# Performance work log

Hardware: AMD Instinct MI355X
Metric: run time of the kernel (lower is better)

Reference implementation:

```python
import jax, jax.numpy as jnp
import numpy as np

N_HEADS = 32
N_KV_HEADS = 8
HEAD_DIM = 64
ROPE_BASE = 10000.0


def _rope(t):
    # t: [b, s, h, d]; Llama-style rotate-half RoPE
    b, s, h, d = t.shape
    inv_freq = 1.0 / (ROPE_BASE ** (jnp.arange(0, d, 2, dtype=jnp.float32) / d))
    freqs = jnp.arange(s, dtype=jnp.float32)[:, None] * inv_freq[None, :]  # [s, d/2]
    cos = jnp.cos(freqs)[None, :, None, :].astype(t.dtype)
    sin = jnp.sin(freqs)[None, :, None, :].astype(t.dtype)
    t1, t2 = t[..., : d // 2], t[..., d // 2 :]
    return jnp.concatenate([t1 * cos - t2 * sin, t2 * cos + t1 * sin], axis=-1)


def setup_inputs() -> dict:
    key = jax.random.key(0)
    ks = jax.random.split(key, 5)
    b, s, d = 2, 2048, 2048
    dkv = d // (N_HEADS // N_KV_HEADS)
    sc = 1.0 / np.sqrt(d)
    return {
        "x": jax.random.normal(ks[0], (b, s, d), jnp.float32),
        "wq": jax.random.normal(ks[1], (d, d), jnp.float32) * sc,
        "wk": jax.random.normal(ks[2], (d, dkv), jnp.float32) * sc,
        "wv": jax.random.normal(ks[3], (d, dkv), jnp.float32) * sc,
        "wo": jax.random.normal(ks[4], (d, d), jnp.float32) * sc,
    }


def reference(x, wq, wk, wv, wo):
    b, s, d = x.shape
    g = N_HEADS // N_KV_HEADS
    q = (x @ wq).reshape(b, s, N_HEADS, HEAD_DIM)
    k = (x @ wk).reshape(b, s, N_KV_HEADS, HEAD_DIM)
    v = (x @ wv).reshape(b, s, N_KV_HEADS, HEAD_DIM)
    q = _rope(q)
    k = _rope(k)
    # GQA: repeat kv heads to match query heads
    k = jnp.repeat(k, g, axis=2)  # [b, s, N_HEADS, d_h]
    v = jnp.repeat(v, g, axis=2)
    scale = 1.0 / np.sqrt(HEAD_DIM)
    scores = jnp.einsum("bqhd,bkhd->bhqk", q, k) * scale  # [b, h, s, s]
    causal = jnp.tril(jnp.ones((s, s), dtype=bool))
    scores = jnp.where(causal[None, None], scores, jnp.finfo(scores.dtype).min)
    probs = jax.nn.softmax(scores, axis=-1)
    out = jnp.einsum("bhqk,bkhd->bqhd", probs, v).reshape(b, s, d)
    return out @ wo
```

## Files before the change

kernel.cpp:

```cpp
#include <hip/hip_runtime.h>
#include <hip/hip_bf16.h>
#include <stdint.h>

typedef __attribute__((ext_vector_type(8))) __bf16 bf16x8;
typedef __attribute__((ext_vector_type(4))) __bf16 bf16x4;
typedef __attribute__((ext_vector_type(4))) float f32x4;

#define QSCALE (0.125f * 1.44269504f)

#define GL16(src, dst) __builtin_amdgcn_global_load_lds( \
    (const __attribute__((address_space(1))) void*)(src), \
    (__attribute__((address_space(3))) void*)(dst), 16, 0, 0)

static __device__ inline unsigned pkbf(float a, float b) {
  __bf16 x = (__bf16)a, y = (__bf16)b;
  unsigned short ux = __builtin_bit_cast(unsigned short, x);
  unsigned short uy = __builtin_bit_cast(unsigned short, y);
  return ((unsigned)uy << 16) | ux;
}

static __device__ inline float ex2(float x) {
#if __has_builtin(__builtin_amdgcn_exp2f)
  return __builtin_amdgcn_exp2f(x);
#else
  float r;
  asm("v_exp_f32 %0, %1" : "=v"(r) : "v"(x));
  return r;
#endif
}

__global__ __launch_bounds__(256) void k_prep(const float* __restrict__ x,
                                              __bf16* __restrict__ xb,
                                              const float* __restrict__ wq,
                                              const float* __restrict__ wk,
                                              const float* __restrict__ wv,
                                              const float* __restrict__ wo,
                                              __bf16* __restrict__ wqkvT,
                                              __bf16* __restrict__ woT,
                                              float* __restrict__ ct,
                                              float* __restrict__ st) {
  int bid = blockIdx.x, tid = threadIdx.x;
  if (bid < 4096) {
    int i = bid * 256 + tid;
    const float4* p = (const float4*)(x) + (size_t)i * 2;
    float4 a = p[0], b = p[1];
    bf16x8 o;
    o[0] = (__bf16)a.x; o[1] = (__bf16)a.y; o[2] = (__bf16)a.z; o[3] = (__bf16)a.w;
    o[4] = (__bf16)b.x; o[5] = (__bf16)b.y; o[6] = (__bf16)b.z; o[7] = (__bf16)b.w;
    ((bf16x8*)xb)[i] = o;
    return;
  }
  if (bid >= 14336) {
    int i = (bid - 14336) * 256 + tid;
    int s = i >> 5, j = i & 31;
    float invf = powf(10000.0f, -(float)j / 32.0f);
    float fr = (float)s * invf;
    ct[i] = cosf(fr);
    st[i] = sinf(fr);
    return;
  }
  __shared__ float tile[32][33];
  const float* w;
  __bf16* wT;
  int N, r;
  if (bid < 8192)       { r = bid - 4096;  w = wq; wT = wqkvT;                        N = 2048; }
  else if (bid < 9216)  { r = bid - 8192;  w = wk; wT = wqkvT + (size_t)2048 * 2048;  N = 512; }
  else if (bid < 10240) { r = bid - 9216;  w = wv; wT = wqkvT + (size_t)2560 * 2048;  N = 512; }
  else                  { r = bid - 10240; w = wo; wT = woT;                          N = 2048; }
  int ntiles = N >> 5;
  int n0 = (r % ntiles) * 32, k0 = (r / ntiles) * 32;
  int tx = tid & 31, ty = tid >> 5;
#pragma unroll
  for (int i = 0; i < 32; i += 8)
    tile[ty + i][tx] = w[(size_t)(k0 + ty + i) * N + n0 + tx];
  __syncthreads();
#pragma unroll
  for (int i = 0; i < 32; i += 8)
    wT[(size_t)(n0 + ty + i) * 2048 + k0 + tx] = (__bf16)tile[tx][ty + i];
}

template <int BN, int NW, int WPN, int MODE>
__global__ __launch_bounds__(NW * 64, NW / 4) void k_gemm256(const __bf16* __restrict__ A,
                                                             const __bf16* __restrict__ BT,
                                                             void* __restrict__ C0,
                                                             __bf16* __restrict__ kb,
                                                             __bf16* __restrict__ vt,
                                                             const float* __restrict__ ct,
                                                             const float* __restrict__ st,
                                                             int K, int NBN) {
  constexpr int WPM = NW / WPN;
  constexpr int MF = 256 / WPM / 16;
  constexpr int NF = BN / WPN / 16;
  constexpr int MH = MF / 2;
  constexpr int CHA = 256 * 8;
  constexpr int CHB = BN * 8;
  constexpr int PA = CHA / (NW * 64);
  constexpr int RA = CHA - PA * NW * 64;
  constexpr int PB = CHB / (NW * 64);
  static_assert(CHB % (NW * 64) == 0, "B chunks must tile threads");
  static_assert(RA % 64 == 0, "A remainder must be wave-aligned");
  static_assert(NF == 4, "epilogue assumes 64-col wave window");
  __shared__ __align__(16) __bf16 lA[2][256 * 64];
  __shared__ __align__(16) __bf16 lB[2][BN * 64];
  int bm = (blockIdx.x / NBN) << 8;
  int bn = (blockIdx.x % NBN) * BN;
  int tid = threadIdx.x, l = tid & 63, w = tid >> 6;
  int wr = w / WPN, wc = w % WPN;
  int lrow = l & 15, lk = l >> 4;
  int NT = K >> 6;
  f32x4 acc[MF][NF] = {};

#define STG(T, BUF)                                                           \
  do {                                                                        \
    int k0_ = (T) << 6;                                                       \
    _Pragma("unroll") for (int i_ = 0; i_ < PA; i_++) {                       \
      int ch_ = i_ * (NW * 64) + tid;                                         \
      int r_ = ch_ >> 3, c_ = ch_ & 7;                                        \
      GL16(A + (size_t)(bm + r_) * K + k0_ + ((c_ ^ (r_ & 7)) << 3),          \
           &lA[BUF][(i_ * (NW * 64) + (w << 6)) * 8]);                        \
    }                                                                         \
    if constexpr (RA > 0) {                                                   \
      if (tid < RA) {                                                         \
        int ch_ = PA * (NW * 64) + tid;                                       \
        int r_ = ch_ >> 3, c_ = ch_ & 7;                                      \
        GL16(A + (size_t)(bm + r_) * K + k0_ + ((c_ ^ (r_ & 7)) << 3),        \
             &lA[BUF][(PA * (NW * 64) + (w << 6)) * 8]);                      \
      }                                                                       \
    }                                                                         \
    _Pragma("unroll") for (int i_ = 0; i_ < PB; i_++) {                       \
      int ch_ = i_ * (NW * 64) + tid;                                         \
      int r_ = ch_ >> 3, c_ = ch_ & 7;                                        \
      GL16(BT + (size_t)(bn + r_) * K + k0_ + ((c_ ^ (r_ & 7)) << 3),         \
           &lB[BUF][(i_ * (NW * 64) + (w << 6)) * 8]);                        \
    }                                                                         \
  } while (0)

#define WAITN()                                                               \
  do {                                                                        \
    if constexpr (RA > 0) {                                                   \
      if (w < (RA >> 6))                                                      \
        asm volatile("s_waitcnt vmcnt(%0)" ::"i"(PA + PB + 1) : "memory");    \
      else                                                                    \
        asm volatile("s_waitcnt vmcnt(%0)" ::"i"(PA + PB) : "memory");        \
    } else {                                                                  \
      asm volatile("s_waitcnt vmcnt(%0)" ::"i"(PA + PB) : "memory");          \
    }                                                                         \
  } while (0)

  STG(0, 0);
  STG(1, 1);
  WAITN();
  __builtin_amdgcn_sched_barrier(0);
  __builtin_amdgcn_s_barrier();

  for (int t = 0; t < NT; t++) {
    int buf = t & 1;
    const char* bA = (const char*)lA[buf];
    const char* bB = (const char*)lB[buf];
    bf16x8 bfr[NF][2], af0[MH][2], af1[MH][2];
#pragma unroll
    for (int nf = 0; nf < NF; nf++) {
      int row = wc * (NF * 16) + nf * 16 + lrow;
#pragma unroll
      for (int kc = 0; kc < 2; kc++)
        bfr[nf][kc] = *(const bf16x8*)(bB + row * 128 +
                                       ((kc * 64 + 16 * lk) ^ ((row & 7) << 4)));
    }
#pragma unroll
    for (int mf = 0; mf < MH; mf++) {
      int row = wr * (MF * 16) + mf * 16 + lrow;
#pragma unroll
      for (int kc = 0; kc < 2; kc++)
        af0[mf][kc] = *(const bf16x8*)(bA + row * 128 +
                                       ((kc * 64 + 16 * lk) ^ ((row & 7) << 4)));
    }
    __builtin_amdgcn_s_setprio(1);
#pragma unroll
    for (int kc = 0; kc < 2; kc++)
#pragma unroll
      for (int mf = 0; mf < MH; mf++)
#pragma unroll
        for (int nf = 0; nf < NF; nf++)
          acc[mf][nf] = __builtin_amdgcn_mfma_f32_16x16x32_bf16(af0[mf][kc], bfr[nf][kc],
                                                                acc[mf][nf], 0, 0, 0);
    __builtin_amdgcn_s_setprio(0);
#pragma unroll
    for (int mf = 0; mf < MH; mf++) {
      int row = wr * (MF * 16) + (MH + mf) * 16 + lrow;
#pragma unroll
      for (int kc = 0; kc < 2; kc++)
        af1[mf][kc] = *(const bf16x8*)(bA + row * 128 +
                                       ((kc * 64 + 16 * lk) ^ ((row & 7) << 4)));
    }
    asm volatile("s_waitcnt lgkmcnt(0)" ::: "memory");
    __builtin_amdgcn_sched_barrier(0);
    __builtin_amdgcn_s_barrier();
    if (t + 2 < NT) STG(t + 2, buf);
    __builtin_amdgcn_s_setprio(1);
#pragma unroll
    for (int kc = 0; kc < 2; kc++)
#pragma unroll
      for (int mf = 0; mf < MH; mf++)
#pragma unroll
        for (int nf = 0; nf < NF; nf++)
          acc[MH + mf][nf] = __builtin_amdgcn_mfma_f32_16x16x32_bf16(
              af1[mf][kc], bfr[nf][kc], acc[MH + mf][nf], 0, 0, 0);
    __builtin_amdgcn_s_setprio(0);
    if (t + 2 < NT) {
      WAITN();
    } else {
      asm volatile("s_waitcnt vmcnt(0)" ::: "memory");
    }
    __builtin_amdgcn_sched_barrier(0);
    __builtin_amdgcn_s_barrier();
  }
#undef STG
#undef WAITN

  if constexpr (MODE == 0) {
    int wcb = bn + wc * 64;
    __bf16* qb = (__bf16*)C0;
    if (wcb < 2048) {
#pragma unroll
      for (int mf = 0; mf < MF; mf++)
#pragma unroll
        for (int r = 0; r < 4; r++) {
          int row = bm + wr * (MF * 16) + mf * 16 + 4 * lk + r;
          int sidx = row & 2047;
#pragma unroll
          for (int nfl = 0; nfl < 2; nfl++) {
            int d = nfl * 16 + lrow;
            float c = ct[sidx * 32 + d], sn = st[sidx * 32 + d];
            float a = acc[mf][nfl][r], b2 = acc[mf][nfl + 2][r];
            qb[(size_t)row * 2048 + wcb + d] = (__bf16)((a * c - b2 * sn) * QSCALE);
            qb[(size_t)row * 2048 + wcb + d + 32] = (__bf16)((b2 * c + a * sn) * QSCALE);
          }
        }
    } else if (wcb < 2560) {
      int cb = wcb - 2048;
#pragma unroll
      for (int mf = 0; mf < MF; mf++)
#pragma unroll
        for (int r = 0; r < 4; r++) {
          int row = bm + wr * (MF * 16) + mf * 16 + 4 * lk + r;
          int sidx = row & 2047;
#pragma unroll
          for (int nfl = 0; nfl < 2; nfl++) {
            int d = nfl * 16 + lrow;
            float c = ct[sidx * 32 + d], sn = st[sidx * 32 + d];
            float a = acc[mf][nfl][r], b2 = acc[mf][nfl + 2][r];
            kb[(size_t)row * 512 + cb + d] = (__bf16)(a * c - b2 * sn);
            kb[(size_t)row * 512 + cb + d + 32] = (__bf16)(b2 * c + a * sn);
          }
        }
    } else {
      int hkk = (wcb - 2560) >> 6;
#pragma unroll
      for (int mf = 0; mf < MF; mf++)
#pragma unroll
        for (int nf = 0; nf < NF; nf++)
#pragma unroll
          for (int r = 0; r < 4; r++) {
            int row = bm + wr * (MF * 16) + mf * 16 + 4 * lk + r;
            int dd = nf * 16 + lrow;
            int bb = row >> 11, s = row & 2047;
            vt[(size_t)(((bb << 3) + hkk) * 64 + dd) * 2048 + s] = (__bf16)acc[mf][nf][r];
          }
    }
  } else {
    float* C = (float*)C0;
#pragma unroll
    for (int mf = 0; mf < MF; mf++)
#pragma unroll
      for (int nf = 0; nf < NF; nf++)
#pragma unroll
        for (int r = 0; r < 4; r++) {
          int row = bm + wr * (MF * 16) + mf * 16 + 4 * lk + r;
          int col = bn + wc * 64 + nf * 16 + lrow;
          C[(size_t)row * 2048 + col] = acc[mf][nf][r];
        }
  }
}

template <int BN, int NW, int WPN, int MODE>
__global__ __launch_bounds__(NW * 64, NW / 4) void k_gemm3d(const __bf16* __restrict__ A,
                                                            const __bf16* __restrict__ BT,
                                                            void* __restrict__ C0,
                                                            int K, int NBN) {
  constexpr int WPM = NW / WPN;
  constexpr int MF = 256 / WPM / 16;
  constexpr int NF = BN / WPN / 16;
  constexpr int MH = MF / 2;
  constexpr int CHA = 256 * 8;
  constexpr int CHB = BN * 8;
  constexpr int PA = CHA / (NW * 64);
  constexpr int RA = CHA - PA * NW * 64;
  constexpr int PB = CHB / (NW * 64);
  static_assert(CHB % (NW * 64) == 0, "B chunks must tile threads");
  static_assert(RA % 64 == 0, "A remainder must be wave-aligned");
  static_assert(NF == 4, "wave owns a 64-col window");
  constexpr int LB = PB;
  constexpr int LA0 = PA + (RA > 0 ? 1 : 0);
  constexpr int LA1 = PA;
  constexpr int NS0 = 2 * LA0 + LB, NS1 = 2 * LA1 + LB;
  constexpr int NM0 = LA0 + LB, NM1 = LA1 + LB;
  __shared__ __align__(16) __bf16 lA[3][256 * 64];
  __shared__ __align__(16) __bf16 lB[2][BN * 64];
  int bid = blockIdx.x;
  int lg = (bid & 7) * ((int)gridDim.x >> 3) + (bid >> 3);
  int bm = (lg / NBN) << 8;
  int bn = (lg % NBN) * BN;
  int tid = threadIdx.x, l = tid & 63, w = tid >> 6;
  int wr = w / WPN, wc = w % WPN;
  int lrow = l & 15, lk = l >> 4;
  int NT = K >> 6;
  f32x4 acc[MF][NF] = {};

#define STGA(T, BUF)                                                          \
  do {                                                                        \
    int k0_ = (T) << 6;                                                       \
    _Pragma("unroll") for (int i_ = 0; i_ < PA; i_++) {                       \
      int ch_ = i_ * (NW * 64) + tid;                                         \
      int r_ = ch_ >> 3, c_ = ch_ & 7;                                        \
      GL16(A + (size_t)(bm + r_) * K + k0_ + ((c_ ^ (r_ & 7)) << 3),          \
           &lA[BUF][(i_ * (NW * 64) + (w << 6)) * 8]);                        \
    }                                                                         \
    if constexpr (RA > 0) {                                                   \
      if (tid < RA) {                                                         \
        int ch_ = PA * (NW * 64) + tid;                                       \
        int r_ = ch_ >> 3, c_ = ch_ & 7;                                      \
        GL16(A + (size_t)(bm + r_) * K + k0_ + ((c_ ^ (r_ & 7)) << 3),        \
             &lA[BUF][(PA * (NW * 64) + (w << 6)) * 8]);                      \
      }                                                                       \
    }                                                                         \
  } while (0)

#define STGB(T, BUF)                                                          \
  do {                                                                        \
    int k0_ = (T) << 6;                                                       \
    _Pragma("unroll") for (int i_ = 0; i_ < PB; i_++) {                       \
      int ch_ = i_ * (NW * 64) + tid;                                         \
      int r_ = ch_ >> 3, c_ = ch_ & 7;                                        \
      GL16(BT + (size_t)(bn + r_) * K + k0_ + ((c_ ^ (r_ & 7)) << 3),         \
           &lB[BUF][(i_ * (NW * 64) + (w << 6)) * 8]);                        \
    }                                                                         \
  } while (0)

#define WAIT_STEADY()                                                         \
  do {                                                                        \
    if constexpr (RA > 0) {                                                   \
      if (w < (RA >> 6))                                                      \
        asm volatile("s_waitcnt vmcnt(%0)" ::"i"(NS0) : "memory");            \
      else                                                                    \
        asm volatile("s_waitcnt vmcnt(%0)" ::"i"(NS1) : "memory");            \
    } else {                                                                  \
      asm volatile("s_waitcnt vmcnt(%0)" ::"i"(NS1) : "memory");              \
    }                                                                         \
  } while (0)

#define WAIT_MID()                                                            \
  do {                                                                        \
    if constexpr (RA > 0) {                                                   \
      if (w < (RA >> 6))                                                      \
        asm volatile("s_waitcnt vmcnt(%0)" ::"i"(NM0) : "memory");            \
      else                                                                    \
        asm volatile("s_waitcnt vmcnt(%0)" ::"i"(NM1) : "memory");            \
    } else {                                                                  \
      asm volatile("s_waitcnt vmcnt(%0)" ::"i"(NM1) : "memory");              \
    }                                                                         \
  } while (0)

  STGB(0, 0); STGA(0, 0);
  STGB(1, 1); STGA(1, 1);
  STGA(2, 2);
  WAIT_STEADY();
  __builtin_amdgcn_sched_barrier(0);
  __builtin_amdgcn_s_barrier();

  int a0 = 0;
  for (int t = 0; t < NT; t++) {
    const char* bA = (const char*)lA[a0];
    const char* bB = (const char*)lB[t & 1];
    bf16x8 bfr[NF][2], af0[MH][2], af1[MH][2];
#pragma unroll
    for (int nf = 0; nf < NF; nf++) {
      int row = wc * (NF * 16) + nf * 16 + lrow;
#pragma unroll
      for (int kc = 0; kc < 2; kc++)
        bfr[nf][kc] = *(const bf16x8*)(bB + row * 128 +
                                       ((kc * 64 + 16 * lk) ^ ((row & 7) << 4)));
    }
#pragma unroll
    for (int mf = 0; mf < MH; mf++) {
      int row = wr * (MF * 16) + mf * 16 + lrow;
#pragma unroll
      for (int kc = 0; kc < 2; kc++)
        af0[mf][kc] = *(const bf16x8*)(bA + row * 128 +
                                       ((kc * 64 + 16 * lk) ^ ((row & 7) << 4)));
    }
#pragma unroll
    for (int mf = 0; mf < MH; mf++) {
      int row = wr * (MF * 16) + (MH + mf) * 16 + lrow;
#pragma unroll
      for (int kc = 0; kc < 2; kc++)
        af1[mf][kc] = *(const bf16x8*)(bA + row * 128 +
                                       ((kc * 64 + 16 * lk) ^ ((row & 7) << 4)));
    }
    __builtin_amdgcn_s_setprio(1);
#pragma unroll
    for (int kc = 0; kc < 2; kc++)
#pragma unroll
      for (int mf = 0; mf < MH; mf++)
#pragma unroll
        for (int nf = 0; nf < NF; nf++)
          acc[mf][nf] = __builtin_amdgcn_mfma_f32_16x16x32_bf16(af0[mf][kc], bfr[nf][kc],
                                                                acc[mf][nf], 0, 0, 0);
    __builtin_amdgcn_s_setprio(0);
    asm volatile("s_waitcnt lgkmcnt(0)" ::: "memory");
    __builtin_amdgcn_sched_barrier(0);
    __builtin_amdgcn_s_barrier();
    if (t + 2 < NT) STGB(t + 2, t & 1);
    if (t + 3 < NT) STGA(t + 3, a0);
    __builtin_amdgcn_s_setprio(1);
#pragma unroll
    for (int kc = 0; kc < 2; kc++)
#pragma unroll
      for (int mf = 0; mf < MH; mf++)
#pragma unroll
        for (int nf = 0; nf < NF; nf++)
          acc[MH + mf][nf] = __builtin_amdgcn_mfma_f32_16x16x32_bf16(
              af1[mf][kc], bfr[nf][kc], acc[MH + mf][nf], 0, 0, 0);
    __builtin_amdgcn_s_setprio(0);
    if (t + 3 < NT) {
      WAIT_STEADY();
    } else if (t + 2 < NT) {
      WAIT_MID();
    } else if (t + 1 < NT) {
      asm volatile("s_waitcnt vmcnt(0)" ::: "memory");
    }
    __builtin_amdgcn_sched_barrier(0);
    __builtin_amdgcn_s_barrier();
    a0 = (a0 == 2) ? 0 : a0 + 1;
  }
#undef STGA
#undef STGB
#undef WAIT_STEADY
#undef WAIT_MID

  float* C = (float*)C0;
#pragma unroll
  for (int mf = 0; mf < MF; mf++)
#pragma unroll
    for (int nf = 0; nf < NF; nf++)
#pragma unroll
      for (int r = 0; r < 4; r++) {
        int row = bm + wr * (MF * 16) + mf * 16 + 4 * lk + r;
        int col = bn + wc * 64 + nf * 16 + lrow;
        C[(size_t)row * 2048 + col] = acc[mf][nf][r];
      }
}

__global__ __launch_bounds__(256, 3) void k_attn(const __bf16* __restrict__ Q,
                                                 const __bf16* __restrict__ Kb,
                                                 const __bf16* __restrict__ VT,
                                                 __bf16* __restrict__ O) {
  __shared__ __align__(16) __bf16 lK[2][64 * 64];
  __shared__ __align__(16) __bf16 lV[2][64 * 64];
  int bid = blockIdx.x;
  int g = bid >> 8, k = (bid >> 4) & 15;
  int c;
  if (g == 0) c = 63 - k;
  else if (g == 1) c = 32 + k;
  else if (g == 2) c = 31 - k;
  else c = k;
  int hk = bid & 7;
  int b = (bid >> 3) & 1;
  int tid = threadIdx.x, l = tid & 63, w = tid >> 6;
  int h = hk * 4 + w;
  int lrow = l & 15, lk = l >> 4;
  int sw = (lrow & 7) << 4;
  int tl = c >> 1;

#define STAGE(BUF, T)                                                                     \
  do {                                                                                    \
    int kv0_ = (T) * 64;                                                                  \
    _Pragma("unroll") for (int i_ = 0; i_ < 2; i_++) {                                    \
      int cb_ = i_ * 256 + w * 64;                                                        \
      int chunk_ = cb_ + l;                                                               \
      int row_ = chunk_ >> 3, cc_ = chunk_ & 7;                                           \
      GL16(Kb + (size_t)(b * 2048 + kv0_ + row_) * 512 + hk * 64 +                        \
               ((cc_ ^ (row_ & 7)) << 3),                                                 \
           &lK[BUF][cb_ * 8]);                                                            \
      GL16(VT + (size_t)((b * 8 + hk) * 64 + row_) * 2048 + kv0_ +                        \
               ((cc_ ^ (row_ & 7)) << 3),                                                 \
           &lV[BUF][cb_ * 8]);                                                            \
    }                                                                                     \
  } while (0)

  bf16x8 aq[2][2];
#pragma unroll
  for (int qf = 0; qf < 2; qf++) {
    int qrow = c * 32 + qf * 16 + lrow;
    const __bf16* qp = Q + (size_t)(b * 2048 + qrow) * 2048 + h * 64 + lk * 8;
    aq[qf][0] = *(const bf16x8*)qp;
    aq[qf][1] = *(const bf16x8*)(qp + 32);
  }
  f32x4 o[2][4] = {};
  float lp[2] = {0.f, 0.f};
  STAGE(0, 0);
  for (int t = 0, buf = 0; t <= tl; t++, buf ^= 1) {
    asm volatile("s_waitcnt vmcnt(0)" ::: "memory");
    __syncthreads();
    if (t < tl) STAGE(buf ^ 1, t + 1);
    const char* K_ = (const char*)lK[buf];
    const char* V_ = (const char*)lV[buf];
    f32x4 s4[2][4];
    __builtin_amdgcn_s_setprio(1);
#pragma unroll
    for (int nf = 0; nf < 4; nf++) {
      const char* kr = K_ + (nf * 16 + lrow) * 128;
      bf16x8 bk0 = *(const bf16x8*)(kr + ((16 * lk) ^ sw));
      bf16x8 bk1 = *(const bf16x8*)(kr + ((64 + 16 * lk) ^ sw));
#pragma unroll
      for (int qf = 0; qf < 2; qf++) {
        f32x4 z = {};
        z = __builtin_amdgcn_mfma_f32_16x16x32_bf16(bk0, aq[qf][0], z, 0, 0, 0);
        z = __builtin_amdgcn_mfma_f32_16x16x32_bf16(bk1, aq[qf][1], z, 0, 0, 0);
        s4[qf][nf] = z;
      }
    }
    __builtin_amdgcn_s_setprio(0);
    if (t == tl) {
      int qo = (c & 1) * 32;
#pragma unroll
      for (int qf = 0; qf < 2; qf++) {
        int qoff = qo + qf * 16 + lrow;
#pragma unroll
        for (int nf = 0; nf < 4; nf++)
#pragma unroll
          for (int r = 0; r < 4; r++)
            if (nf * 16 + 4 * lk + r > qoff) s4[qf][nf][r] = -1e30f;
      }
    }
#pragma unroll
    for (int qf = 0; qf < 2; qf++) {
      float ps = 0.f;
#pragma unroll
      for (int nf = 0; nf < 4; nf++)
#pragma unroll
        for (int r = 0; r < 4; r++) {
          float pv = ex2(s4[qf][nf][r]);
          s4[qf][nf][r] = pv;
          ps += pv;
        }
      lp[qf] += ps;
    }
    __builtin_amdgcn_s_setprio(1);
#pragma unroll
    for (int np = 0; np < 2; np++) {
      bf16x8 pb[2];
#pragma unroll
      for (int qf = 0; qf < 2; qf++) {
        uint4 t4;
        t4.x = pkbf(s4[qf][np][0], s4[qf][np][1]);
        t4.y = pkbf(s4[qf][np][2], s4[qf][np][3]);
        t4.z = pkbf(s4[qf][np + 2][0], s4[qf][np + 2][1]);
        t4.w = pkbf(s4[qf][np + 2][2], s4[qf][np + 2][3]);
        pb[qf] = __builtin_bit_cast(bf16x8, t4);
      }
#pragma unroll
      for (int dn = 0; dn < 4; dn++) {
        const char* vr = V_ + (dn * 16 + lrow) * 128;
        uint2 a0 = *(const uint2*)(vr + ((np * 32 + 8 * lk) ^ sw));
        uint2 a1 = *(const uint2*)(vr + (((np + 2) * 32 + 8 * lk) ^ sw));
        uint4 av;
        av.x = a0.x; av.y = a0.y; av.z = a1.x; av.w = a1.y;
        bf16x8 va = __builtin_bit_cast(bf16x8, av);
#pragma unroll
        for (int qf = 0; qf < 2; qf++)
          o[qf][dn] = __builtin_amdgcn_mfma_f32_16x16x32_bf16(va, pb[qf], o[qf][dn], 0, 0, 0);
      }
    }
    __builtin_amdgcn_s_setprio(0);
  }
#pragma unroll
  for (int qf = 0; qf < 2; qf++) {
    float s = lp[qf];
    s += __shfl_xor(s, 16);
    s += __shfl_xor(s, 32);
    float inv = 1.f / s;
    int qrow = c * 32 + qf * 16 + lrow;
    __bf16* op = O + (size_t)(b * 2048 + qrow) * 2048 + h * 64 + 4 * lk;
#pragma unroll
    for (int dn = 0; dn < 4; dn++) {
      bf16x4 stv;
#pragma unroll
      for (int r = 0; r < 4; r++) stv[r] = (__bf16)(o[qf][dn][r] * inv);
      *(bf16x4*)(op + dn * 16) = stv;
    }
  }
#undef STAGE
}

extern "C" void kernel_launch(void* const* d_in, const int* in_sizes, int n_in,
                              void* d_out, int out_size, void* d_ws, size_t ws_size,
                              hipStream_t stream) {
  const float* x = (const float*)d_in[0];
  const float* wq = (const float*)d_in[1];
  const float* wk = (const float*)d_in[2];
  const float* wv = (const float*)d_in[3];
  const float* wo = (const float*)d_in[4];
  char* ws = (char*)d_ws;
  __bf16* xb    = (__bf16*)(ws + 0);
  __bf16* wqkvT = (__bf16*)(ws + 16777216);
  __bf16* woT   = (__bf16*)(ws + 29360128);
  __bf16* qb    = (__bf16*)(ws + 37748736);
  __bf16* kb    = (__bf16*)(ws + 54525952);
  __bf16* vt    = (__bf16*)(ws + 58720256);
  __bf16* ob    = (__bf16*)(ws + 62914560);
  float*  ct    = (float*)(ws + 79691776);
  float*  st    = (float*)(ws + 79953920);
  float* out = (float*)d_out;

  k_prep<<<14592, 256, 0, stream>>>(x, xb, wq, wk, wv, wo, wqkvT, woT, ct, st);
  k_gemm256<192, 12, 3, 0><<<256, 768, 0, stream>>>(xb, wqkvT, qb, kb, vt, ct, st, 2048, 16);
  k_attn<<<1024, 256, 0, stream>>>(qb, kb, vt, ob);
  k_gemm3d<128, 8, 2, 1><<<256, 512, 0, stream>>>(ob, woT, out, 2048, 16);
}
```

Before: 162.3 us.

## Fuse fp32-to-bf16 conversion of x into QKV GEMM A-tile loads

```diff
diff --git a/kernel.cpp b/kernel.cpp
--- a/kernel.cpp
+++ b/kernel.cpp
@@ -29,9 +29,7 @@
 #endif
 }
 
-__global__ __launch_bounds__(256) void k_prep(const float* __restrict__ x,
-                                              __bf16* __restrict__ xb,
-                                              const float* __restrict__ wq,
+__global__ __launch_bounds__(256) void k_prep(const float* __restrict__ wq,
                                               const float* __restrict__ wk,
                                               const float* __restrict__ wv,
                                               const float* __restrict__ wo,
@@ -40,18 +38,8 @@
                                               float* __restrict__ ct,
                                               float* __restrict__ st) {
   int bid = blockIdx.x, tid = threadIdx.x;
-  if (bid < 4096) {
-    int i = bid * 256 + tid;
-    const float4* p = (const float4*)(x) + (size_t)i * 2;
-    float4 a = p[0], b = p[1];
-    bf16x8 o;
-    o[0] = (__bf16)a.x; o[1] = (__bf16)a.y; o[2] = (__bf16)a.z; o[3] = (__bf16)a.w;
-    o[4] = (__bf16)b.x; o[5] = (__bf16)b.y; o[6] = (__bf16)b.z; o[7] = (__bf16)b.w;
-    ((bf16x8*)xb)[i] = o;
-    return;
-  }
-  if (bid >= 14336) {
-    int i = (bid - 14336) * 256 + tid;
+  if (bid >= 10240) {
+    int i = (bid - 10240) * 256 + tid;
     int s = i >> 5, j = i & 31;
     float invf = powf(10000.0f, -(float)j / 32.0f);
     float fr = (float)s * invf;
@@ -63,10 +51,10 @@
   const float* w;
   __bf16* wT;
   int N, r;
-  if (bid < 8192)       { r = bid - 4096;  w = wq; wT = wqkvT;                        N = 2048; }
-  else if (bid < 9216)  { r = bid - 8192;  w = wk; wT = wqkvT + (size_t)2048 * 2048;  N = 512; }
-  else if (bid < 10240) { r = bid - 9216;  w = wv; wT = wqkvT + (size_t)2560 * 2048;  N = 512; }
-  else                  { r = bid - 10240; w = wo; wT = woT;                          N = 2048; }
+  if (bid < 4096)       { r = bid;         w = wq; wT = wqkvT;                        N = 2048; }
+  else if (bid < 5120)  { r = bid - 4096;  w = wk; wT = wqkvT + (size_t)2048 * 2048;  N = 512; }
+  else if (bid < 6144)  { r = bid - 5120;  w = wv; wT = wqkvT + (size_t)2560 * 2048;  N = 512; }
+  else                  { r = bid - 6144;  w = wo; wT = woT;                          N = 2048; }
   int ntiles = N >> 5;
   int n0 = (r % ntiles) * 32, k0 = (r / ntiles) * 32;
   int tx = tid & 31, ty = tid >> 5;
@@ -79,27 +67,17 @@
     wT[(size_t)(n0 + ty + i) * 2048 + k0 + tx] = (__bf16)tile[tx][ty + i];
 }
 
-template <int BN, int NW, int WPN, int MODE>
-__global__ __launch_bounds__(NW * 64, NW / 4) void k_gemm256(const __bf16* __restrict__ A,
-                                                             const __bf16* __restrict__ BT,
-                                                             void* __restrict__ C0,
-                                                             __bf16* __restrict__ kb,
-                                                             __bf16* __restrict__ vt,
-                                                             const float* __restrict__ ct,
-                                                             const float* __restrict__ st,
-                                                             int K, int NBN) {
-  constexpr int WPM = NW / WPN;
-  constexpr int MF = 256 / WPM / 16;
-  constexpr int NF = BN / WPN / 16;
-  constexpr int MH = MF / 2;
-  constexpr int CHA = 256 * 8;
-  constexpr int CHB = BN * 8;
-  constexpr int PA = CHA / (NW * 64);
-  constexpr int RA = CHA - PA * NW * 64;
-  constexpr int PB = CHB / (NW * 64);
-  static_assert(CHB % (NW * 64) == 0, "B chunks must tile threads");
-  static_assert(RA % 64 == 0, "A remainder must be wave-aligned");
-  static_assert(NF == 4, "epilogue assumes 64-col wave window");
+__global__ __launch_bounds__(768, 3) void k_gemmqkv(const float* __restrict__ X,
+                                                    const __bf16* __restrict__ BT,
+                                                    __bf16* __restrict__ qb,
+                                                    __bf16* __restrict__ kb,
+                                                    __bf16* __restrict__ vt,
+                                                    const float* __restrict__ ct,
+                                                    const float* __restrict__ st,
+                                                    int K, int NBN) {
+  constexpr int BN = 192, WPN = 3;
+  constexpr int MF = 4, NF = 4, MH = 2;
+  constexpr int PB = BN * 8 / 768;
   __shared__ __align__(16) __bf16 lA[2][256 * 64];
   __shared__ __align__(16) __bf16 lB[2][BN * 64];
   int bm = (blockIdx.x / NBN) << 8;
@@ -110,51 +88,57 @@
   int NT = K >> 6;
   f32x4 acc[MF][NF] = {};
 
-#define STG(T, BUF)                                                           \
+  int ch0 = tid, ch1 = 768 + tid, ch2 = 1536 + tid;
+  bool has2 = (tid < 512);
+
+#define ALOAD(dst, ch, T)                                                     \
+  do {                                                                        \
+    const float4* p_ = (const float4*)(X + (size_t)(bm + ((ch) >> 3)) * K +   \
+                                       ((T) << 6) +                           \
+                                       ((((ch) & 7) ^ (((ch) >> 3) & 7)) << 3)); \
+    (dst)[0] = p_[0];                                                         \
+    (dst)[1] = p_[1];                                                         \
+  } while (0)
+
+#define ACVT(src, ch, BUF)                                                    \
+  do {                                                                        \
+    bf16x8 o_;                                                                \
+    o_[0] = (__bf16)(src)[0].x; o_[1] = (__bf16)(src)[0].y;                   \
+    o_[2] = (__bf16)(src)[0].z; o_[3] = (__bf16)(src)[0].w;                   \
+    o_[4] = (__bf16)(src)[1].x; o_[5] = (__bf16)(src)[1].y;                   \
+    o_[6] = (__bf16)(src)[1].z; o_[7] = (__bf16)(src)[1].w;                   \
+    *(bf16x8*)((char*)lA[BUF] + (size_t)(ch) * 16) = o_;                      \
+  } while (0)
+
+#define STGB(T, BUF)                                                          \
   do {                                                                        \
     int k0_ = (T) << 6;                                                       \
-    _Pragma("unroll") for (int i_ = 0; i_ < PA; i_++) {                       \
-      int ch_ = i_ * (NW * 64) + tid;                                         \
-      int r_ = ch_ >> 3, c_ = ch_ & 7;                                        \
-      GL16(A + (size_t)(bm + r_) * K + k0_ + ((c_ ^ (r_ & 7)) << 3),          \
-           &lA[BUF][(i_ * (NW * 64) + (w << 6)) * 8]);                        \
-    }                                                                         \
-    if constexpr (RA > 0) {                                                   \
-      if (tid < RA) {                                                         \
-        int ch_ = PA * (NW * 64) + tid;                                       \
-        int r_ = ch_ >> 3, c_ = ch_ & 7;                                      \
-        GL16(A + (size_t)(bm + r_) * K + k0_ + ((c_ ^ (r_ & 7)) << 3),        \
-             &lA[BUF][(PA * (NW * 64) + (w << 6)) * 8]);                      \
-      }                                                                       \
-    }                                                                         \
     _Pragma("unroll") for (int i_ = 0; i_ < PB; i_++) {                       \
-      int ch_ = i_ * (NW * 64) + tid;                                         \
+      int ch_ = i_ * 768 + tid;                                               \
       int r_ = ch_ >> 3, c_ = ch_ & 7;                                        \
       GL16(BT + (size_t)(bn + r_) * K + k0_ + ((c_ ^ (r_ & 7)) << 3),         \
-           &lB[BUF][(i_ * (NW * 64) + (w << 6)) * 8]);                        \
+           &lB[BUF][(i_ * 768 + (w << 6)) * 8]);                              \
     }                                                                         \
   } while (0)
 
-#define WAITN()                                                               \
-  do {                                                                        \
-    if constexpr (RA > 0) {                                                   \
-      if (w < (RA >> 6))                                                      \
-        asm volatile("s_waitcnt vmcnt(%0)" ::"i"(PA + PB + 1) : "memory");    \
-      else                                                                    \
-        asm volatile("s_waitcnt vmcnt(%0)" ::"i"(PA + PB) : "memory");        \
-    } else {                                                                  \
-      asm volatile("s_waitcnt vmcnt(%0)" ::"i"(PA + PB) : "memory");          \
-    }                                                                         \
-  } while (0)
-
-  STG(0, 0);
-  STG(1, 1);
-  WAITN();
+  float4 p0[2], p1[2], p2[2];
+  ALOAD(p0, ch0, 0); ALOAD(p1, ch1, 0); if (has2) ALOAD(p2, ch2, 0);
+  asm volatile("s_waitcnt vmcnt(0)" ::: "memory");
+  ACVT(p0, ch0, 0); ACVT(p1, ch1, 0); if (has2) ACVT(p2, ch2, 0);
+  ALOAD(p0, ch0, 1); ALOAD(p1, ch1, 1); if (has2) ALOAD(p2, ch2, 1);
+  STGB(0, 0); STGB(1, 1);
+  asm volatile("s_waitcnt vmcnt(4)" ::: "memory");
+  ACVT(p0, ch0, 1); ACVT(p1, ch1, 1); if (has2) ACVT(p2, ch2, 1);
+  asm volatile("s_waitcnt vmcnt(2) lgkmcnt(0)" ::: "memory");
   __builtin_amdgcn_sched_barrier(0);
   __builtin_amdgcn_s_barrier();
 
   for (int t = 0; t < NT; t++) {
     int buf = t & 1;
+    if (t + 2 < NT) {
+      ALOAD(p0, ch0, t + 2); ALOAD(p1, ch1, t + 2); if (has2) ALOAD(p2, ch2, t + 2);
+      __builtin_amdgcn_sched_barrier(0);
+    }
     const char* bA = (const char*)lA[buf];
     const char* bB = (const char*)lB[buf];
     bf16x8 bfr[NF][2], af0[MH][2], af1[MH][2];
@@ -195,7 +179,13 @@
     asm volatile("s_waitcnt lgkmcnt(0)" ::: "memory");
     __builtin_amdgcn_sched_barrier(0);
     __builtin_amdgcn_s_barrier();
-    if (t + 2 < NT) STG(t + 2, buf);
+    if (t + 2 < NT) {
+      STGB(t + 2, buf);
+      asm volatile("s_waitcnt vmcnt(2)" ::: "memory");
+      ACVT(p0, ch0, buf); ACVT(p1, ch1, buf); if (has2) ACVT(p2, ch2, buf);
+    } else {
+      asm volatile("s_waitcnt vmcnt(0)" ::: "memory");
+    }
     __builtin_amdgcn_s_setprio(1);
 #pragma unroll
     for (int kc = 0; kc < 2; kc++)
@@ -206,78 +196,59 @@
           acc[MH + mf][nf] = __builtin_amdgcn_mfma_f32_16x16x32_bf16(
               af1[mf][kc], bfr[nf][kc], acc[MH + mf][nf], 0, 0, 0);
     __builtin_amdgcn_s_setprio(0);
-    if (t + 2 < NT) {
-      WAITN();
-    } else {
-      asm volatile("s_waitcnt vmcnt(0)" ::: "memory");
-    }
     __builtin_amdgcn_sched_barrier(0);
     __builtin_amdgcn_s_barrier();
   }
-#undef STG
-#undef WAITN
-
-  if constexpr (MODE == 0) {
-    int wcb = bn + wc * 64;
-    __bf16* qb = (__bf16*)C0;
-    if (wcb < 2048) {
-#pragma unroll
-      for (int mf = 0; mf < MF; mf++)
+#undef ALOAD
+#undef ACVT
+#undef STGB
+
+  int wcb = bn + wc * 64;
+  if (wcb < 2048) {
+#pragma unroll
+    for (int mf = 0; mf < MF; mf++)
+#pragma unroll
+      for (int r = 0; r < 4; r++) {
+        int row = bm + wr * (MF * 16) + mf * 16 + 4 * lk + r;
+        int sidx = row & 2047;
+#pragma unroll
+        for (int nfl = 0; nfl < 2; nfl++) {
+          int d = nfl * 16 + lrow;
+          float c = ct[sidx * 32 + d], sn = st[sidx * 32 + d];
+          float a = acc[mf][nfl][r], b2 = acc[mf][nfl + 2][r];
+          qb[(size_t)row * 2048 + wcb + d] = (__bf16)((a * c - b2 * sn) * QSCALE);
+          qb[(size_t)row * 2048 + wcb + d + 32] = (__bf16)((b2 * c + a * sn) * QSCALE);
+        }
+      }
+  } else if (wcb < 2560) {
+    int cb = wcb - 2048;
+#pragma unroll
+    for (int mf = 0; mf < MF; mf++)
+#pragma unroll
+      for (int r = 0; r < 4; r++) {
+        int row = bm + wr * (MF * 16) + mf * 16 + 4 * lk + r;
+        int sidx = row & 2047;
+#pragma unroll
+        for (int nfl = 0; nfl < 2; nfl++) {
+          int d = nfl * 16 + lrow;
+          float c = ct[sidx * 32 + d], sn = st[sidx * 32 + d];
+          float a = acc[mf][nfl][r], b2 = acc[mf][nfl + 2][r];
+          kb[(size_t)row * 512 + cb + d] = (__bf16)(a * c - b2 * sn);
+          kb[(size_t)row * 512 + cb + d + 32] = (__bf16)(b2 * c + a * sn);
+        }
+      }
+  } else {
+    int hkk = (wcb - 2560) >> 6;
+#pragma unroll
+    for (int mf = 0; mf < MF; mf++)
+#pragma unroll
+      for (int nf = 0; nf < NF; nf++)
 #pragma unroll
         for (int r = 0; r < 4; r++) {
           int row = bm + wr * (MF * 16) + mf * 16 + 4 * lk + r;
-          int sidx = row & 2047;
-#pragma unroll
-          for (int nfl = 0; nfl < 2; nfl++) {
-            int d = nfl * 16 + lrow;
-            float c = ct[sidx * 32 + d], sn = st[sidx * 32 + d];
-            float a = acc[mf][nfl][r], b2 = acc[mf][nfl + 2][r];
-            qb[(size_t)row * 2048 + wcb + d] = (__bf16)((a * c - b2 * sn) * QSCALE);
-            qb[(size_t)row * 2048 + wcb + d + 32] = (__bf16)((b2 * c + a * sn) * QSCALE);
-          }
-        }
-    } else if (wcb < 2560) {
-      int cb = wcb - 2048;
-#pragma unroll
-      for (int mf = 0; mf < MF; mf++)
-#pragma unroll
-        for (int r = 0; r < 4; r++) {
-          int row = bm + wr * (MF * 16) + mf * 16 + 4 * lk + r;
-          int sidx = row & 2047;
-#pragma unroll
-          for (int nfl = 0; nfl < 2; nfl++) {
-            int d = nfl * 16 + lrow;
-            float c = ct[sidx * 32 + d], sn = st[sidx * 32 + d];
-            float a = acc[mf][nfl][r], b2 = acc[mf][nfl + 2][r];
-            kb[(size_t)row * 512 + cb + d] = (__bf16)(a * c - b2 * sn);
-            kb[(size_t)row * 512 + cb + d + 32] = (__bf16)(b2 * c + a * sn);
-          }
-        }
-    } else {
-      int hkk = (wcb - 2560) >> 6;
-#pragma unroll
-      for (int mf = 0; mf < MF; mf++)
-#pragma unroll
-        for (int nf = 0; nf < NF; nf++)
-#pragma unroll
-          for (int r = 0; r < 4; r++) {
-            int row = bm + wr * (MF * 16) + mf * 16 + 4 * lk + r;
-            int dd = nf * 16 + lrow;
-            int bb = row >> 11, s = row & 2047;
-            vt[(size_t)(((bb << 3) + hkk) * 64 + dd) * 2048 + s] = (__bf16)acc[mf][nf][r];
-          }
-    }
-  } else {
-    float* C = (float*)C0;
-#pragma unroll
-    for (int mf = 0; mf < MF; mf++)
-#pragma unroll
-      for (int nf = 0; nf < NF; nf++)
-#pragma unroll
-        for (int r = 0; r < 4; r++) {
-          int row = bm + wr * (MF * 16) + mf * 16 + 4 * lk + r;
-          int col = bn + wc * 64 + nf * 16 + lrow;
-          C[(size_t)row * 2048 + col] = acc[mf][nf][r];
+          int dd = nf * 16 + lrow;
+          int bb = row >> 11, s = row & 2047;
+          vt[(size_t)(((bb << 3) + hkk) * 64 + dd) * 2048 + s] = (__bf16)acc[mf][nf][r];
         }
   }
 }
@@ -467,12 +438,7 @@
   __shared__ __align__(16) __bf16 lK[2][64 * 64];
   __shared__ __align__(16) __bf16 lV[2][64 * 64];
   int bid = blockIdx.x;
-  int g = bid >> 8, k = (bid >> 4) & 15;
-  int c;
-  if (g == 0) c = 63 - k;
-  else if (g == 1) c = 32 + k;
-  else if (g == 2) c = 31 - k;
-  else c = k;
+  int c = 63 - (bid >> 4);
   int hk = bid & 7;
   int b = (bid >> 3) & 1;
   int tid = threadIdx.x, l = tid & 63, w = tid >> 6;
@@ -611,7 +577,6 @@
   const float* wv = (const float*)d_in[3];
   const float* wo = (const float*)d_in[4];
   char* ws = (char*)d_ws;
-  __bf16* xb    = (__bf16*)(ws + 0);
   __bf16* wqkvT = (__bf16*)(ws + 16777216);
   __bf16* woT   = (__bf16*)(ws + 29360128);
   __bf16* qb    = (__bf16*)(ws + 37748736);
@@ -622,8 +587,8 @@
   float*  st    = (float*)(ws + 79953920);
   float* out = (float*)d_out;
 
-  k_prep<<<14592, 256, 0, stream>>>(x, xb, wq, wk, wv, wo, wqkvT, woT, ct, st);
-  k_gemm256<192, 12, 3, 0><<<256, 768, 0, stream>>>(xb, wqkvT, qb, kb, vt, ct, st, 2048, 16);
+  k_prep<<<10496, 256, 0, stream>>>(wq, wk, wv, wo, wqkvT, woT, ct, st);
+  k_gemmqkv<<<256, 768, 0, stream>>>(x, wqkvT, qb, kb, vt, ct, st, 2048, 16);
   k_attn<<<1024, 256, 0, stream>>>(qb, kb, vt, ob);
   k_gemm3d<128, 8, 2, 1><<<256, 512, 0, stream>>>(ob, woT, out, 2048, 16);
 }
```

After: 178.1 us. +9.7%, slower.
